# Optimization experiments

Hardware: AMD Instinct MI355X
Metric: run time of the kernel (lower is better)

## Reference

```python
import jax, jax.numpy as jnp
import numpy as np

BITS = 32
N = 2_000_000

# Soft logic gates on {0,1}-valued floats (matching the SNN gate modules)
# xor(a,b) = a + b - 2ab ; not(x) = 1 - x ; and(a,b) = a*b ; or(a,b) = a + b - ab

def setup_inputs() -> dict:
    key = jax.random.key(0)
    kA, kB = jax.random.split(key)
    A = jax.random.randint(kA, (N, BITS), 0, 2).astype(jnp.float32)
    B = jax.random.randint(kB, (N, BITS), 0, 2).astype(jnp.float32)
    return {"A": A, "B": B}


def reference(A, B):
    # A, B: [..., bits], MSB first, values in {0,1}
    xor_all = A + B - 2.0 * A * B          # VecXOR
    eq_all = 1.0 - xor_all                  # VecNOT(xor)
    not_b = 1.0 - B                         # VecNOT(B)
    gt_all = A * not_b                      # VecAND -> A_i AND (NOT B_i)

    # a_eq_b: AND-tree over all bits
    a_eq_b = jnp.prod(eq_all, axis=-1, keepdims=True)

    # eq_prefix_i = AND of eq[0..i-1]; prefix_0 = 1 (no constraint for MSB)
    eq_cum = jnp.cumprod(eq_all, axis=-1)                      # [..., bits]
    prefix = jnp.concatenate(
        [jnp.ones_like(eq_cum[..., :1]), eq_cum[..., :-1]], axis=-1
    )                                                          # [..., bits]

    # term_i = prefix_i AND gt_i ; a_gt_b = OR over i of term_i
    # chained soft-OR of binary terms == 1 - prod(1 - term_i)
    terms = prefix * gt_all
    a_gt_b = 1.0 - jnp.prod(1.0 - terms, axis=-1, keepdims=True)

    return (a_gt_b, a_eq_b)
```

## Files before the change

### kernel.cpp

```cpp
#include <hip/hip_runtime.h>
#include <hip/hip_bf16.h>


__global__ void __launch_bounds__(256)
comparator_kernel(const float4* __restrict__ A, const float4* __restrict__ B,
                  float* __restrict__ out_gt, float* __restrict__ out_eq,
                  long long nRows) {
    const long long base = (long long)blockIdx.x * 512 + threadIdx.x;
    const long long i0 = base;
    const long long i1 = base + 256;

    float4 a0 = A[i0];
    float4 b0 = B[i0];
    float4 a1 = A[i1];
    float4 b1 = B[i1];

#define PACK(v) (((unsigned)((v).x > 0.5f) << 3) | ((unsigned)((v).y > 0.5f) << 2) | \
                 ((unsigned)((v).z > 0.5f) << 1) |  (unsigned)((v).w > 0.5f))
    unsigned an0 = PACK(a0), bn0 = PACK(b0);
    unsigned an1 = PACK(a1), bn1 = PACK(b1);
#undef PACK

    unsigned long long d0 = __ballot(an0 != bn0);
    unsigned long long t0 = __ballot(an0 > bn0);
    unsigned long long d1 = __ballot(an1 != bn1);
    unsigned long long t1 = __ballot(an1 > bn1);

    const int lane = threadIdx.x & 63;
    if (lane < 16) {
        const int g = lane & 7;
        const bool second = lane >= 8;
        unsigned long long d = second ? d1 : d0;
        unsigned long long t = second ? t1 : t0;
        unsigned db = (unsigned)(d >> (8 * g)) & 0xFFu;
        unsigned tb = (unsigned)(t >> (8 * g)) & 0xFFu;

        const long long waveRow0 = ((long long)blockIdx.x * 512 + (threadIdx.x & 192)) >> 3;
        const long long row = waveRow0 + g + (second ? 32 : 0);

        if (row < nRows) {
            unsigned msdiff = db & (0u - db);
            out_gt[row] = (tb & msdiff) ? 1.0f : 0.0f;
            out_eq[row] = (db == 0u)   ? 1.0f : 0.0f;
        }
    }
}

extern "C" void kernel_launch(void* const* d_in, const int* in_sizes, int n_in,
                              void* d_out, int out_size, void* d_ws, size_t ws_size,
                              hipStream_t stream) {
    const float4* A = (const float4*)d_in[0];
    const float4* B = (const float4*)d_in[1];
    float* out = (float*)d_out;

    const int BITS = 32;
    long long n = in_sizes[0] / BITS;

    float* out_gt = out;
    float* out_eq = out + n;

    long long totalVec = n * 8;
    long long grid = (totalVec + 511) / 512;
    comparator_kernel<<<(int)grid, 256, 0, stream>>>(A, B, out_gt, out_eq, n);
}
```

Baseline: 482.9 us.

## Use persistent grid-stride loop with register double-buffered prefetch of tiles

Replaces the one-tile-per-block launch with a fixed grid of 3125 blocks. Each block loops over tiles and prefetches the next tile's A/B float4 loads into registers while it packs, ballots and writes the current tile. This is meant to cut block launch and scheduling overhead and keep more loads in flight on a purely bandwidth-bound kernel. It doubles the register footprint and drops the row<nRows bounds check, which relies on nTiles covering rows exactly.

```diff
diff --git a/kernel.cpp b/kernel.cpp
--- a/kernel.cpp
+++ b/kernel.cpp
@@ -5,45 +5,56 @@
 __global__ void __launch_bounds__(256)
 comparator_kernel(const float4* __restrict__ A, const float4* __restrict__ B,
                   float* __restrict__ out_gt, float* __restrict__ out_eq,
-                  long long nRows) {
-    const long long base = (long long)blockIdx.x * 512 + threadIdx.x;
-    const long long i0 = base;
-    const long long i1 = base + 256;
-
-    float4 a0 = A[i0];
-    float4 b0 = B[i0];
-    float4 a1 = A[i1];
-    float4 b1 = B[i1];
+                  int nTiles) {
+    const int tid = threadIdx.x;
+    const int lane = tid & 63;
 
 #define PACK(v) (((unsigned)((v).x > 0.5f) << 3) | ((unsigned)((v).y > 0.5f) << 2) | \
                  ((unsigned)((v).z > 0.5f) << 1) |  (unsigned)((v).w > 0.5f))
-    unsigned an0 = PACK(a0), bn0 = PACK(b0);
-    unsigned an1 = PACK(a1), bn1 = PACK(b1);
-#undef PACK
 
-    unsigned long long d0 = __ballot(an0 != bn0);
-    unsigned long long t0 = __ballot(an0 > bn0);
-    unsigned long long d1 = __ballot(an1 != bn1);
-    unsigned long long t1 = __ballot(an1 > bn1);
+    int t = blockIdx.x;
+    long long base = (long long)t * 512 + tid;
+    float4 a0 = A[base], b0 = B[base];
+    float4 a1 = A[base + 256], b1 = B[base + 256];
 
-    const int lane = threadIdx.x & 63;
-    if (lane < 16) {
-        const int g = lane & 7;
-        const bool second = lane >= 8;
-        unsigned long long d = second ? d1 : d0;
-        unsigned long long t = second ? t1 : t0;
-        unsigned db = (unsigned)(d >> (8 * g)) & 0xFFu;
-        unsigned tb = (unsigned)(t >> (8 * g)) & 0xFFu;
+    for (;;) {
+        const int tn = t + gridDim.x;
+        const bool more = tn < nTiles;
+        float4 na0, nb0, na1, nb1;
+        if (more) {
+            long long nb = (long long)tn * 512 + tid;
+            na0 = A[nb];  nb0 = B[nb];
+            na1 = A[nb + 256];  nb1 = B[nb + 256];
+        }
 
-        const long long waveRow0 = ((long long)blockIdx.x * 512 + (threadIdx.x & 192)) >> 3;
-        const long long row = waveRow0 + g + (second ? 32 : 0);
+        unsigned an0 = PACK(a0), bn0 = PACK(b0);
+        unsigned an1 = PACK(a1), bn1 = PACK(b1);
 
-        if (row < nRows) {
+        unsigned long long d0 = __ballot(an0 != bn0);
+        unsigned long long g0 = __ballot(an0 > bn0);
+        unsigned long long d1 = __ballot(an1 != bn1);
+        unsigned long long g1 = __ballot(an1 > bn1);
+
+        if (lane < 16) {
+            const int g = lane & 7;
+            const bool second = lane >= 8;
+            unsigned long long d = second ? d1 : d0;
+            unsigned long long gm = second ? g1 : g0;
+            unsigned db = (unsigned)(d >> (8 * g)) & 0xFFu;
+            unsigned tb = (unsigned)(gm >> (8 * g)) & 0xFFu;
+
+            const long long row =
+                (((long long)t * 512 + (tid & 192)) >> 3) + g + (second ? 32 : 0);
             unsigned msdiff = db & (0u - db);
             out_gt[row] = (tb & msdiff) ? 1.0f : 0.0f;
             out_eq[row] = (db == 0u)   ? 1.0f : 0.0f;
         }
+
+        if (!more) break;
+        t = tn;
+        a0 = na0; b0 = nb0; a1 = na1; b1 = nb1;
     }
+#undef PACK
 }
 
 extern "C" void kernel_launch(void* const* d_in, const int* in_sizes, int n_in,
@@ -60,6 +71,7 @@
     float* out_eq = out + n;
 
     long long totalVec = n * 8;
-    long long grid = (totalVec + 511) / 512;
-    comparator_kernel<<<(int)grid, 256, 0, stream>>>(A, B, out_gt, out_eq, n);
+    int nTiles = (int)((totalVec + 511) / 512);
+    int grid = 3125;
+    comparator_kernel<<<grid, 256, 0, stream>>>(A, B, out_gt, out_eq, nTiles);
 }
```

New measurement: 492.0 us. Within noise of the previous version (+1.9%).
